# Kernel tuning notes

Hardware: AMD Instinct MI355X
Metric: run time of the kernel (lower is better)

The kernel has to match this reference:

```python
import jax, jax.numpy as jnp
import numpy as np

BITS = 4
NPACK = 32 // BITS            # 8 nibbles per int32
GROUPSIZE = 128
IN_F = 8192
OUT_F = 8192
BATCH = 64
NGROUPS = IN_F // GROUPSIZE   # 64
MASK = (1 << BITS) - 1        # 15


def setup_inputs() -> dict:
    key = jax.random.key(0)
    k1, k2, k3, k4, k5 = jax.random.split(key, 5)
    x = jax.random.normal(k1, (BATCH, IN_F), dtype=jnp.float32)
    qweight = jax.random.randint(k2, (IN_F // NPACK, OUT_F), 0, 2**31 - 1, dtype=jnp.int32)
    qzeros = jax.random.randint(k3, (NGROUPS, OUT_F // NPACK), 0, 2**31 - 1, dtype=jnp.int32)
    scales = jax.random.uniform(k4, (NGROUPS, OUT_F), dtype=jnp.float32, minval=1e-3, maxval=1e-2)
    bias = jax.random.normal(k5, (OUT_F,), dtype=jnp.float32)
    return {"x": x, "qweight": qweight, "qzeros": qzeros, "scales": scales, "bias": bias}


def _dequantize(qweight, qzeros, scales):
    shifts = (jnp.arange(NPACK, dtype=jnp.int32) * BITS)
    # unpack weight nibbles along in_features: [in/8, 8, out] -> [in, out]
    w = (qweight[:, None, :] >> shifts[None, :, None]) & MASK
    w = w.reshape(IN_F, OUT_F).astype(jnp.float32)
    # unpack zero points along out_features: [g, out/8, 8] -> [g, out]
    zp = (qzeros[:, :, None] >> shifts[None, None, :]) & MASK
    zp = zp.reshape(NGROUPS, OUT_F) + 1                       # optimum format stores zp-1
    zp = jnp.where(zp > MASK, 0, zp).astype(jnp.float32)      # wraparound per recover()
    g_idx = jnp.arange(IN_F) // GROUPSIZE                     # per-input-channel group id
    return (w - zp[g_idx]) * scales[g_idx]                    # [in, out] fp weight


def reference(x, qweight, qzeros, scales, bias):
    W = _dequantize(qweight, qzeros, scales)                  # [in, out]
    return x @ W + bias                                       # F.linear(x, W.T, bias)
```

## Files before the change

### kernel.cpp

```cpp
#include <hip/hip_runtime.h>
#include <hip/hip_bf16.h>

#define IN_F 8192
#define OUT_F 8192
#define BATCH 64
#define KSPLIT 8

typedef __attribute__((ext_vector_type(8))) short  bf16x8_t;
typedef __attribute__((ext_vector_type(8))) ushort u16x8_t;
typedef __attribute__((ext_vector_type(4))) float  f32x4_t;

__global__ void __launch_bounds__(512, 4)
wol_mfma(const float*  __restrict__ x,
         const int*    __restrict__ qw,
         const int*    __restrict__ qz,
         const float*  __restrict__ sc,
         ushort*       __restrict__ part) {
    const int nt   = blockIdx.x & 31;
    const int ks   = blockIdx.x >> 5;
    const int wid  = threadIdx.x >> 6;
    const int lane = threadIdx.x & 63;
    const int ln   = lane & 15;
    const int kb   = lane >> 4;
    const int colbase = nt * 256 + wid * 32;
    const int k0      = ks * 1024;
    const int gbase   = k0 >> 7;
    const int qrowb   = k0 >> 3;

    unsigned qc[4][2]; float svc[2]; unsigned zwc[2];
#pragma unroll
    for (int kt = 0; kt < 4; ++kt)
#pragma unroll
        for (int nj = 0; nj < 2; ++nj)
            qc[kt][nj] = (unsigned)qw[(size_t)(qrowb + kt * 4 + kb) * OUT_F +
                                      colbase + nj * 16 + ln];
#pragma unroll
    for (int nj = 0; nj < 2; ++nj) {
        const int c = colbase + nj * 16 + ln;
        svc[nj] = sc[gbase * OUT_F + c];
        zwc[nj] = (unsigned)qz[gbase * (OUT_F / 8) + (c >> 3)];
    }
    __builtin_amdgcn_sched_barrier(0);

    __shared__ ushort lds_x[128 * 64 * 8];
    {
#pragma unroll
        for (int i = 0; i < 16; ++i) {
            const int idx = i * 512 + (int)threadIdx.x;
            const int row = idx >> 7;
            const int k8l = idx & 127;
            const float4* sp = (const float4*)&x[(size_t)row * IN_F + k0 + k8l * 8];
            const float4 a = sp[0], b = sp[1];
            const float f[8] = {a.x, a.y, a.z, a.w, b.x, b.y, b.z, b.w};
            union { ushort u[8]; bf16x8_t v; } o;
#pragma unroll
            for (int j = 0; j < 8; ++j) {
                __hip_bfloat16 hb = __float2bfloat16(f[j]);
                o.u[j] = *reinterpret_cast<ushort*>(&hb);
            }
            unsigned byteoff = (unsigned)(row * 2048 + k8l * 16);
            byteoff ^= (unsigned)((row & 7) << 4);
            *(bf16x8_t*)((char*)lds_x + byteoff) = o.v;
        }
    }
    __syncthreads();

    const unsigned xorv = (unsigned)((ln & 7) << 4);

    f32x4_t acc[4][2];
#pragma unroll
    for (int mi = 0; mi < 4; ++mi)
#pragma unroll
        for (int nj = 0; nj < 2; ++nj) acc[mi][nj] = (f32x4_t)0.0f;

#pragma unroll 1
    for (int g = 0; g < 8; ++g) {
        unsigned qn[4][2]; float svn[2]; unsigned zwn[2];
        if (g < 7) {
            const int qrow1 = qrowb + (g + 1) * 16;
#pragma unroll
            for (int kt = 0; kt < 4; ++kt)
#pragma unroll
                for (int nj = 0; nj < 2; ++nj)
                    qn[kt][nj] = (unsigned)qw[(size_t)(qrow1 + kt * 4 + kb) * OUT_F +
                                              colbase + nj * 16 + ln];
#pragma unroll
            for (int nj = 0; nj < 2; ++nj) {
                const int c = colbase + nj * 16 + ln;
                svn[nj] = sc[(gbase + g + 1) * OUT_F + c];
                zwn[nj] = (unsigned)qz[(gbase + g + 1) * (OUT_F / 8) + (c >> 3)];
            }
            __builtin_amdgcn_sched_barrier(0);
        }

        float s[2], dz[2];
#pragma unroll
        for (int nj = 0; nj < 2; ++nj) {
            const unsigned zp = ((zwc[nj] >> ((ln & 7) * 4)) + 1u) & 15u;
            s[nj]  = svc[nj];
            dz[nj] = -(float)zp * svc[nj];
        }

#pragma unroll
        for (int kt = 0; kt < 4; ++kt) {
            const unsigned kbyte = (unsigned)(g * 256 + kt * 64 + kb * 16) ^ xorv;
            bf16x8_t af[4];
#pragma unroll
            for (int mi = 0; mi < 4; ++mi)
                af[mi] = *(const bf16x8_t*)((const char*)lds_x +
                            (unsigned)((mi * 16 + ln) * 2048) + kbyte);
#pragma unroll
            for (int nj = 0; nj < 2; ++nj) {
                const unsigned qv  = qc[kt][nj];
                const unsigned qlo = qv & 0x0F0F0F0Fu;
                const unsigned qhi = (qv >> 4) & 0x0F0F0F0Fu;
                union { ushort u[8]; bf16x8_t v; } bu;
#pragma unroll
                for (int b = 0; b < 4; ++b) {
                    const float fe = (float)((qlo >> (8 * b)) & 0xFFu);
                    const float fo = (float)((qhi >> (8 * b)) & 0xFFu);
                    const float we = fe * s[nj] + dz[nj];
                    const float wo = fo * s[nj] + dz[nj];
                    __hip_bfloat16 he = __float2bfloat16(we);
                    __hip_bfloat16 ho = __float2bfloat16(wo);
                    bu.u[2 * b]     = *reinterpret_cast<ushort*>(&he);
                    bu.u[2 * b + 1] = *reinterpret_cast<ushort*>(&ho);
                }
#pragma unroll
                for (int mi = 0; mi < 4; ++mi)
                    acc[mi][nj] = __builtin_amdgcn_mfma_f32_16x16x32_bf16(
                        af[mi], bu.v, acc[mi][nj], 0, 0, 0);
            }
        }

        if (g < 7) {
#pragma unroll
            for (int kt = 0; kt < 4; ++kt)
#pragma unroll
                for (int nj = 0; nj < 2; ++nj) qc[kt][nj] = qn[kt][nj];
#pragma unroll
            for (int nj = 0; nj < 2; ++nj) { svc[nj] = svn[nj]; zwc[nj] = zwn[nj]; }
        }
    }

    union { ushort u[32]; u16x8_t v8[4]; } ob;
#pragma unroll
    for (int mi = 0; mi < 4; ++mi)
#pragma unroll
        for (int nj = 0; nj < 2; ++nj)
#pragma unroll
            for (int j = 0; j < 4; ++j) {
                __hip_bfloat16 h = __float2bfloat16(acc[mi][nj][j]);
                ob.u[(mi * 2 + nj) * 4 + j] = *reinterpret_cast<ushort*>(&h);
            }
    u16x8_t* pb = (u16x8_t*)part + ((size_t)(ks * 32 + nt) * 512 + threadIdx.x) * 4;
#pragma unroll
    for (int i = 0; i < 4; ++i) pb[i] = ob.v8[i];
}

__global__ void __launch_bounds__(256)
wol_reduce(const ushort* __restrict__ part,
           const float*  __restrict__ bias,
           float* __restrict__ out) {
    const int u   = blockIdx.x * 256 + threadIdx.x;
    const int v8  = u & 3;
    const int tid = (u >> 2) & 511;
    const int nt  = u >> 11;

    float s[8];
#pragma unroll
    for (int e = 0; e < 8; ++e) s[e] = 0.0f;
#pragma unroll
    for (int ks = 0; ks < KSPLIT; ++ks) {
        const u16x8_t p = *((const u16x8_t*)part +
                            (((size_t)(ks * 32 + nt) * 512 + tid) * 4 + v8));
#pragma unroll
        for (int e = 0; e < 8; ++e) {
            union { unsigned b; float f; } cv;
            cv.b = ((unsigned)(ushort)p[e]) << 16;
            s[e] += cv.f;
        }
    }

    const int wid = tid >> 6, lane = tid & 63;
    const int ln = lane & 15, kb = lane >> 4;
#pragma unroll
    for (int e = 0; e < 8; ++e) {
        const int idx = v8 * 8 + e;
        const int mi = idx >> 3, nj = (idx >> 2) & 1, j = idx & 3;
        const int row = mi * 16 + kb * 4 + j;
        const int col = nt * 256 + wid * 32 + nj * 16 + ln;
        out[(size_t)row * OUT_F + col] = s[e] + bias[col];
    }
}

extern "C" void kernel_launch(void* const* d_in, const int* in_sizes, int n_in,
                              void* d_out, int out_size, void* d_ws, size_t ws_size,
                              hipStream_t stream) {
    const float* x    = (const float*)d_in[0];
    const int*   qw   = (const int*)d_in[1];
    const int*   qz   = (const int*)d_in[2];
    const float* sc   = (const float*)d_in[3];
    const float* bias = (const float*)d_in[4];
    float* out = (float*)d_out;

    ushort* prt = (ushort*)d_ws;

    (void)in_sizes; (void)n_in; (void)ws_size; (void)out_size;

    wol_mfma<<<256, 512, 0, stream>>>(x, qw, qz, sc, prt);
    wol_reduce<<<256, 256, 0, stream>>>(prt, bias, out);
}
```

Before: 26.82 us.

## Split block waves across K halves with wider column tiles and LDS reduction

```diff
diff --git a/kernel.cpp b/kernel.cpp
--- a/kernel.cpp
+++ b/kernel.cpp
@@ -10,7 +10,7 @@
 typedef __attribute__((ext_vector_type(8))) ushort u16x8_t;
 typedef __attribute__((ext_vector_type(4))) float  f32x4_t;
 
-__global__ void __launch_bounds__(512, 4)
+__global__ void __launch_bounds__(512, 2)
 wol_mfma(const float*  __restrict__ x,
          const int*    __restrict__ qw,
          const int*    __restrict__ qz,
@@ -22,23 +22,26 @@
     const int lane = threadIdx.x & 63;
     const int ln   = lane & 15;
     const int kb   = lane >> 4;
-    const int colbase = nt * 256 + wid * 32;
+    const int cg   = wid & 3;
+    const int kg   = wid >> 2;
+    const int colbase = nt * 256 + cg * 64;
     const int k0      = ks * 1024;
-    const int gbase   = k0 >> 7;
-    const int qrowb   = k0 >> 3;
-
-    unsigned qc[4][2]; float svc[2]; unsigned zwc[2];
+    const int kwave   = k0 + kg * 512;
+    const int gbaseW  = kwave >> 7;
+    const int qrowbW  = kwave >> 3;
+
+    unsigned qc[4][4]; float svc[4]; unsigned zwc[4];
 #pragma unroll
     for (int kt = 0; kt < 4; ++kt)
 #pragma unroll
-        for (int nj = 0; nj < 2; ++nj)
-            qc[kt][nj] = (unsigned)qw[(size_t)(qrowb + kt * 4 + kb) * OUT_F +
+        for (int nj = 0; nj < 4; ++nj)
+            qc[kt][nj] = (unsigned)qw[(size_t)(qrowbW + kt * 4 + kb) * OUT_F +
                                       colbase + nj * 16 + ln];
 #pragma unroll
-    for (int nj = 0; nj < 2; ++nj) {
+    for (int nj = 0; nj < 4; ++nj) {
         const int c = colbase + nj * 16 + ln;
-        svc[nj] = sc[gbase * OUT_F + c];
-        zwc[nj] = (unsigned)qz[gbase * (OUT_F / 8) + (c >> 3)];
+        svc[nj] = sc[gbaseW * OUT_F + c];
+        zwc[nj] = (unsigned)qz[gbaseW * (OUT_F / 8) + (c >> 3)];
     }
     __builtin_amdgcn_sched_barrier(0);
 
@@ -67,35 +70,35 @@
 
     const unsigned xorv = (unsigned)((ln & 7) << 4);
 
-    f32x4_t acc[4][2];
+    f32x4_t acc[4][4];
 #pragma unroll
     for (int mi = 0; mi < 4; ++mi)
 #pragma unroll
-        for (int nj = 0; nj < 2; ++nj) acc[mi][nj] = (f32x4_t)0.0f;
+        for (int nj = 0; nj < 4; ++nj) acc[mi][nj] = (f32x4_t)0.0f;
 
 #pragma unroll 1
-    for (int g = 0; g < 8; ++g) {
-        unsigned qn[4][2]; float svn[2]; unsigned zwn[2];
-        if (g < 7) {
-            const int qrow1 = qrowb + (g + 1) * 16;
+    for (int g = 0; g < 4; ++g) {
+        unsigned qn[4][4]; float svn[4]; unsigned zwn[4];
+        if (g < 3) {
+            const int qrow1 = qrowbW + (g + 1) * 16;
 #pragma unroll
             for (int kt = 0; kt < 4; ++kt)
 #pragma unroll
-                for (int nj = 0; nj < 2; ++nj)
+                for (int nj = 0; nj < 4; ++nj)
                     qn[kt][nj] = (unsigned)qw[(size_t)(qrow1 + kt * 4 + kb) * OUT_F +
                                               colbase + nj * 16 + ln];
 #pragma unroll
-            for (int nj = 0; nj < 2; ++nj) {
+            for (int nj = 0; nj < 4; ++nj) {
                 const int c = colbase + nj * 16 + ln;
-                svn[nj] = sc[(gbase + g + 1) * OUT_F + c];
-                zwn[nj] = (unsigned)qz[(gbase + g + 1) * (OUT_F / 8) + (c >> 3)];
+                svn[nj] = sc[(gbaseW + g + 1) * OUT_F + c];
+                zwn[nj] = (unsigned)qz[(gbaseW + g + 1) * (OUT_F / 8) + (c >> 3)];
             }
             __builtin_amdgcn_sched_barrier(0);
         }
 
-        float s[2], dz[2];
-#pragma unroll
-        for (int nj = 0; nj < 2; ++nj) {
+        float s[4], dz[4];
+#pragma unroll
+        for (int nj = 0; nj < 4; ++nj) {
             const unsigned zp = ((zwc[nj] >> ((ln & 7) * 4)) + 1u) & 15u;
             s[nj]  = svc[nj];
             dz[nj] = -(float)zp * svc[nj];
@@ -103,14 +106,15 @@
 
 #pragma unroll
         for (int kt = 0; kt < 4; ++kt) {
-            const unsigned kbyte = (unsigned)(g * 256 + kt * 64 + kb * 16) ^ xorv;
+            const unsigned kbyte =
+                (unsigned)((kg * 64 + g * 16 + kt * 4 + kb) * 16) ^ xorv;
             bf16x8_t af[4];
 #pragma unroll
             for (int mi = 0; mi < 4; ++mi)
                 af[mi] = *(const bf16x8_t*)((const char*)lds_x +
                             (unsigned)((mi * 16 + ln) * 2048) + kbyte);
 #pragma unroll
-            for (int nj = 0; nj < 2; ++nj) {
+            for (int nj = 0; nj < 4; ++nj) {
                 const unsigned qv  = qc[kt][nj];
                 const unsigned qlo = qv & 0x0F0F0F0Fu;
                 const unsigned qhi = (qv >> 4) & 0x0F0F0F0Fu;
@@ -133,39 +137,56 @@
             }
         }
 
-        if (g < 7) {
+        if (g < 3) {
 #pragma unroll
             for (int kt = 0; kt < 4; ++kt)
 #pragma unroll
-                for (int nj = 0; nj < 2; ++nj) qc[kt][nj] = qn[kt][nj];
-#pragma unroll
-            for (int nj = 0; nj < 2; ++nj) { svc[nj] = svn[nj]; zwc[nj] = zwn[nj]; }
-        }
-    }
-
-    union { ushort u[32]; u16x8_t v8[4]; } ob;
+                for (int nj = 0; nj < 4; ++nj) qc[kt][nj] = qn[kt][nj];
+#pragma unroll
+            for (int nj = 0; nj < 4; ++nj) { svc[nj] = svn[nj]; zwc[nj] = zwn[nj]; }
+        }
+    }
+
+    __syncthreads();
+    float* red = (float*)lds_x;
+    if (kg == 1) {
+#pragma unroll
+        for (int mi = 0; mi < 4; ++mi)
+#pragma unroll
+            for (int nj = 0; nj < 4; ++nj)
+                *(f32x4_t*)&red[(cg * 64 + lane) * 68 + (mi * 4 + nj) * 4] =
+                    acc[mi][nj];
+    }
+    __syncthreads();
+    if (kg == 1) return;
+
+    union { ushort u[64]; u16x8_t v8[8]; } ob;
 #pragma unroll
     for (int mi = 0; mi < 4; ++mi)
 #pragma unroll
-        for (int nj = 0; nj < 2; ++nj)
+        for (int nj = 0; nj < 4; ++nj) {
+            const f32x4_t r =
+                *(const f32x4_t*)&red[(cg * 64 + lane) * 68 + (mi * 4 + nj) * 4];
 #pragma unroll
             for (int j = 0; j < 4; ++j) {
-                __hip_bfloat16 h = __float2bfloat16(acc[mi][nj][j]);
-                ob.u[(mi * 2 + nj) * 4 + j] = *reinterpret_cast<ushort*>(&h);
-            }
-    u16x8_t* pb = (u16x8_t*)part + ((size_t)(ks * 32 + nt) * 512 + threadIdx.x) * 4;
-#pragma unroll
-    for (int i = 0; i < 4; ++i) pb[i] = ob.v8[i];
+                const float v = acc[mi][nj][j] + r[j];
+                __hip_bfloat16 h = __float2bfloat16(v);
+                ob.u[(mi * 4 + nj) * 4 + j] = *reinterpret_cast<ushort*>(&h);
+            }
+        }
+    u16x8_t* pb = (u16x8_t*)part + ((size_t)(ks * 32 + nt) * 256 + threadIdx.x) * 8;
+#pragma unroll
+    for (int i = 0; i < 8; ++i) pb[i] = ob.v8[i];
 }
 
 __global__ void __launch_bounds__(256)
 wol_reduce(const ushort* __restrict__ part,
            const float*  __restrict__ bias,
            float* __restrict__ out) {
-    const int u   = blockIdx.x * 256 + threadIdx.x;
-    const int v8  = u & 3;
-    const int tid = (u >> 2) & 511;
-    const int nt  = u >> 11;
+    const int u    = blockIdx.x * 256 + threadIdx.x;
+    const int v8   = u & 7;
+    const int tidA = (u >> 3) & 255;
+    const int nt   = u >> 11;
 
     float s[8];
 #pragma unroll
@@ -173,7 +194,7 @@
 #pragma unroll
     for (int ks = 0; ks < KSPLIT; ++ks) {
         const u16x8_t p = *((const u16x8_t*)part +
-                            (((size_t)(ks * 32 + nt) * 512 + tid) * 4 + v8));
+                            (((size_t)(ks * 32 + nt) * 256 + tidA) * 8 + v8));
 #pragma unroll
         for (int e = 0; e < 8; ++e) {
             union { unsigned b; float f; } cv;
@@ -182,14 +203,14 @@
         }
     }
 
-    const int wid = tid >> 6, lane = tid & 63;
+    const int cg = tidA >> 6, lane = tidA & 63;
     const int ln = lane & 15, kb = lane >> 4;
 #pragma unroll
     for (int e = 0; e < 8; ++e) {
         const int idx = v8 * 8 + e;
-        const int mi = idx >> 3, nj = (idx >> 2) & 1, j = idx & 3;
+        const int mi = idx >> 4, nj = (idx >> 2) & 3, j = idx & 3;
         const int row = mi * 16 + kb * 4 + j;
-        const int col = nt * 256 + wid * 32 + nj * 16 + ln;
+        const int col = nt * 256 + cg * 64 + nj * 16 + ln;
         out[(size_t)row * OUT_F + col] = s[e] + bias[col];
     }
 }
```

Result: slower. 30.08 us (+12.1%).
